# Optimization experiments

Measured on AMD Instinct MI355X. Metric: run time of the kernel, lower is better.

The kernel has to match this reference:

```python
import jax, jax.numpy as jnp
import numpy as np

N = 50000
E = 800000
F_IN = 256
HID = 96
N_CLS = 32
NEG_SLOPE = 0.2


def setup_inputs() -> dict:
    key = jax.random.key(0)
    ks = jax.random.split(key, 10)
    x = jax.random.normal(ks[0], (N, F_IN), dtype=jnp.float32)
    edge_index = jax.random.randint(ks[1], (2, E), 0, N, dtype=jnp.int64)
    s1 = 1.0 / np.sqrt(F_IN)
    s2 = 1.0 / np.sqrt(HID)
    return {
        "x": x,
        "edge_index": edge_index,
        "W1": jax.random.normal(ks[2], (F_IN, HID), dtype=jnp.float32) * s1,
        "a1_src": jax.random.normal(ks[3], (HID,), dtype=jnp.float32) * s2,
        "a1_dst": jax.random.normal(ks[4], (HID,), dtype=jnp.float32) * s2,
        "b1": jnp.zeros((HID,), dtype=jnp.float32),
        "W2": jax.random.normal(ks[5], (HID, N_CLS), dtype=jnp.float32) * s2,
        "a2_src": jax.random.normal(ks[6], (N_CLS,), dtype=jnp.float32) * (1.0 / np.sqrt(N_CLS)),
        "a2_dst": jax.random.normal(ks[7], (N_CLS,), dtype=jnp.float32) * (1.0 / np.sqrt(N_CLS)),
        "b2": jnp.zeros((N_CLS,), dtype=jnp.float32),
    }


def _gat_conv(x, src, dst, W, a_src, a_dst, b, n_nodes):
    # single-head GATConv (PyG defaults), self-loops already in src/dst
    h = x @ W                                  # [N, out]
    alpha_src = h @ a_src                      # [N]
    alpha_dst = h @ a_dst                      # [N]
    e = alpha_src[src] + alpha_dst[dst]        # [E'] edge logits (msg j->i: dst groups)
    e = jnp.where(e > 0, e, NEG_SLOPE * e)     # leaky_relu
    # segment softmax over edges grouped by destination node
    m = jax.ops.segment_max(e, dst, num_segments=n_nodes)
    ex = jnp.exp(e - m[dst])
    denom = jax.ops.segment_sum(ex, dst, num_segments=n_nodes)
    alpha = ex / denom[dst]                    # [E']
    out = jax.ops.segment_sum(alpha[:, None] * h[src], dst, num_segments=n_nodes)
    return out + b


def reference(x, edge_index, W1, a1_src, a1_dst, b1, W2, a2_src, a2_dst, b2):
    loops = jnp.arange(N, dtype=edge_index.dtype)
    src = jnp.concatenate([edge_index[0], loops])
    dst = jnp.concatenate([edge_index[1], loops])
    h = _gat_conv(x, src, dst, W1, a1_src, a1_dst, b1, N)
    h = jax.nn.elu(h)
    # dropout omitted (eval mode, training=False)
    out = _gat_conv(h, src, dst, W2, a2_src, a2_dst, b2, N)
    return jax.nn.log_softmax(out, axis=1)
```

## Files before the change

kernel.cpp:

```cpp
#include <hip/hip_runtime.h>
#include <cstdint>
#include <cstddef>

#define NNODES 50000
#define NEDGES 800000
#define MEDGES (NEDGES + NNODES)
#define FIN    256
#define HID    96
#define NCLS   32
#define NEG_SLOPE 0.2f

#define NBUCK  391
#define BCAP   3072

typedef unsigned int uint32;
typedef __attribute__((ext_vector_type(8))) short short8;
typedef __attribute__((ext_vector_type(4))) float f32x4;

__device__ __forceinline__ ushort bf_round(float f) {
    uint32 u = __float_as_uint(f);
    u += 0x7FFFu + ((u >> 16) & 1u);
    return (ushort)(u >> 16);
}
__device__ __forceinline__ uint32 pack_bf16x2(float a, float b) {
    return (uint32)bf_round(a) | ((uint32)bf_round(b) << 16);
}
__device__ __forceinline__ float bf_lo(uint32 u) { return __uint_as_float(u << 16); }
__device__ __forceinline__ float bf_hi(uint32 u) { return __uint_as_float(u & 0xFFFF0000u); }
__device__ __forceinline__ float lrelu(float t) { return (t > 0.f) ? t : NEG_SLOPE * t; }
__device__ __forceinline__ float af(int i) { return __int_as_float(i); }
__device__ __forceinline__ float elu_fast(float t) { return (t > 0.f) ? t : (__expf(t) - 1.f); }


__global__ __launch_bounds__(256) void packw_kernel(const float* __restrict__ W1,
                                                    ushort* __restrict__ W1p,
                                                    int* __restrict__ gcount) {
    int stride = gridDim.x * 256;
    for (int idx = blockIdx.x * 256 + threadIdx.x; idx < NBUCK; idx += stride)
        gcount[idx] = 0;
    for (int idx = blockIdx.x * 256 + threadIdx.x; idx < 6 * 8 * 64 * 8; idx += stride) {
        int j     = idx & 7;
        int lane  = (idx >> 3) & 63;
        int kstep = (idx >> 9) & 7;
        int ntile = idx >> 12;
        int k = kstep * 32 + ((lane >> 4) << 3) + j;
        int n = ntile * 16 + (lane & 15);
        W1p[idx] = bf_round(W1[(size_t)k * 96 + n]);
    }
}


__global__ __launch_bounds__(256) void bucket1_kernel(const int* __restrict__ ei,
                                                      int* __restrict__ gcount,
                                                      int* __restrict__ staging) {
    __shared__ int hist[NBUCK];
    __shared__ int base_sh[NBUCK];
    for (int i = threadIdx.x; i < NBUCK; i += 256) hist[i] = 0;
    __syncthreads();

    int v[8], rk[8], bk[8];
    int e0 = blockIdx.x * 2048;
#pragma unroll
    for (int i = 0; i < 8; ++i) {
        int e = e0 + i * 256 + threadIdx.x;
        if (e < MEDGES) {
            int s, d;
            if (e < NEDGES) { s = ei[e]; d = ei[NEDGES + e]; }
            else            { s = e - NEDGES; d = s; }
            bk[i] = d >> 7;
            v[i]  = s | ((d & 127) << 16);
            rk[i] = atomicAdd(&hist[bk[i]], 1);
        } else bk[i] = -1;
    }
    __syncthreads();
    for (int i = threadIdx.x; i < NBUCK; i += 256) {
        int c = hist[i];
        base_sh[i] = c ? atomicAdd(&gcount[i], c) : 0;
    }
    __syncthreads();
#pragma unroll
    for (int i = 0; i < 8; ++i) {
        if (bk[i] >= 0) {
            int pos = base_sh[bk[i]] + rk[i];
            if (pos < BCAP)
                staging[(size_t)bk[i] * BCAP + pos] = v[i];
        }
    }
}


__global__ __launch_bounds__(256) void b2gemm1_kernel(const int* __restrict__ staging,
                                                      const int* __restrict__ gcount,
                                                      int* __restrict__ rowptr,
                                                      int* __restrict__ esrc,
                                                      const float* __restrict__ x,
                                                      const ushort* __restrict__ W1p,
                                                      const float* __restrict__ a_src,
                                                      const float* __restrict__ a_dst,
                                                      ushort* __restrict__ h1,
                                                      float* __restrict__ as1,
                                                      float* __restrict__ ad1) {
    __shared__ int dcount[128];
    __shared__ int dincl[128];
    __shared__ int dexcl[128];
    __shared__ int fillc[128];
    __shared__ int red_s[256];

    if (blockIdx.x < NBUCK) {
        const int b = blockIdx.x;
        const int t = threadIdx.x;

        int pv = 0;
        for (int idx = t; idx < b; idx += 256) pv += gcount[idx];
        red_s[t] = pv;
        __syncthreads();
        for (int off2 = 128; off2; off2 >>= 1) {
            if (t < off2) red_s[t] += red_s[t + off2];
            __syncthreads();
        }
        const int ebase = red_s[0];
        const int cnt   = gcount[b];
        const int node0 = b << 7;
        const int* st   = staging + (size_t)b * BCAP;

        for (int i = t; i < 128; i += 256) { dcount[i] = 0; fillc[i] = 0; }
        __syncthreads();

        for (int i = t; i < cnt; i += 256)
            atomicAdd(&dcount[st[i] >> 16], 1);
        __syncthreads();

        if (t < 128) dincl[t] = dcount[t];
        __syncthreads();
        for (int off = 1; off < 128; off <<= 1) {
            int val = (t >= off && t < 128) ? dincl[t - off] : 0;
            __syncthreads();
            if (t < 128) dincl[t] += val;
            __syncthreads();
        }
        if (t < 128) {
            int excl = dincl[t] - dcount[t];
            dexcl[t] = excl;
            int node = node0 + t;
            if (node < NNODES) rowptr[node] = ebase + excl;
        }
        if (b == NBUCK - 1 && t == 0) rowptr[NNODES] = MEDGES;
        __syncthreads();

        for (int i = t; i < cnt; i += 256) {
            int v = st[i];
            int dd = v >> 16;
            int r = atomicAdd(&fillc[dd], 1);
            esrc[ebase + dexcl[dd] + r] = v & 0xFFFF;
        }
        return;
    }

    const int tid  = threadIdx.x;
    const int lane = tid & 63;
    const int wv   = tid >> 6;
    const int m    = lane & 15;
    const int quad = lane >> 4;
    const int node0 = (blockIdx.x - NBUCK) * 64;

    int arow = node0 + wv * 16 + m;
    if (arow >= NNODES) arow = NNODES - 1;
    const float* xr = x + (size_t)arow * FIN + quad * 8;

    const short8* Wp = (const short8*)W1p;

    f32x4 acc[6];
#pragma unroll
    for (int t = 0; t < 6; ++t) acc[t] = (f32x4){0.f, 0.f, 0.f, 0.f};

#pragma unroll
    for (int ks = 0; ks < 8; ++ks) {
        float4 v0 = *(const float4*)(xr + ks * 32);
        float4 v1 = *(const float4*)(xr + ks * 32 + 4);
        short8 a;
        a[0] = (short)bf_round(v0.x); a[1] = (short)bf_round(v0.y);
        a[2] = (short)bf_round(v0.z); a[3] = (short)bf_round(v0.w);
        a[4] = (short)bf_round(v1.x); a[5] = (short)bf_round(v1.y);
        a[6] = (short)bf_round(v1.z); a[7] = (short)bf_round(v1.w);
#pragma unroll
        for (int t = 0; t < 6; ++t) {
            short8 b = Wp[(t * 8 + ks) * 64 + lane];
            acc[t] = __builtin_amdgcn_mfma_f32_16x16x32_bf16(a, b, acc[t], 0, 0, 0);
        }
    }

    float as_reg[6], ad_reg[6];
#pragma unroll
    for (int t = 0; t < 6; ++t) {
        as_reg[t] = a_src[t * 16 + m];
        ad_reg[t] = a_dst[t * 16 + m];
    }

#pragma unroll
    for (int r = 0; r < 4; ++r) {
        int node = node0 + wv * 16 + quad * 4 + r;
        float ps = 0.f, pd = 0.f;
#pragma unroll
        for (int t = 0; t < 6; ++t) {
            ps += acc[t][r] * as_reg[t];
            pd += acc[t][r] * ad_reg[t];
        }
#pragma unroll
        for (int off = 1; off < 16; off <<= 1) {
            ps += __shfl_xor(ps, off);
            pd += __shfl_xor(pd, off);
        }
        if (node < NNODES) {
            ushort* hp = h1 + (size_t)node * 96 + m;
#pragma unroll
            for (int t = 0; t < 6; ++t) hp[t * 16] = bf_round(acc[t][r]);
            if (m == 0) { as1[node] = ps; ad1[node] = pd; }
        }
    }
}


__global__ __launch_bounds__(256) void agg96g2_kernel(const ushort* __restrict__ h,
                                                      const float* __restrict__ asrc,
                                                      const float* __restrict__ adst,
                                                      const float* __restrict__ bias,
                                                      const int* __restrict__ rowptr,
                                                      const int* __restrict__ esrc,
                                                      const float* __restrict__ W2,
                                                      const float* __restrict__ a2s,
                                                      const float* __restrict__ a2d,
                                                      uint32* __restrict__ h2b,
                                                      float* __restrict__ as2,
                                                      float* __restrict__ ad2) {
    __shared__ int2 sa[4][2][32];
    __shared__ __align__(16) float W2t[32 * 100];
    __shared__ __align__(16) float y_sh[4][2][96];

    for (int idx = threadIdx.x; idx < 96 * 32; idx += 256) {
        int c = idx & 31, k = idx >> 5;
        W2t[c * 100 + k] = W2[idx];
    }
    __syncthreads();

    const int wave = threadIdx.x >> 6;
    const int lane = threadIdx.x & 63;
    const int hf   = lane >> 5;
    const int fl32 = lane & 31;
    const int i = blockIdx.x * 8 + wave * 2 + hf;

    const int start = rowptr[i];
    const int deg   = rowptr[i + 1] - start;
    const float ad  = adst[i];
    const float a2s_v = a2s[fl32];
    const float a2d_v = a2d[fl32];
    const int fl    = (fl32 < 24) ? fl32 : 23;

    float acc0 = 0.f, acc1 = 0.f, acc2 = 0.f, acc3 = 0.f;

    if (deg <= 32) {
        bool valid = fl32 < deg;
        int s_reg = valid ? esrc[start + fl32] : 0;
        float e = valid ? lrelu(asrc[s_reg] + ad) : -1e30f;
        float mx = e;
#pragma unroll
        for (int off = 16; off; off >>= 1) mx = fmaxf(mx, __shfl_xor(mx, off));
        float ex = valid ? __expf(e - mx) : 0.f;
        float sum = ex;
#pragma unroll
        for (int off = 16; off; off >>= 1) sum += __shfl_xor(sum, off);
        sa[wave][hf][fl32] = make_int2(s_reg, __float_as_int(ex / sum));

        const int4* sap = (const int4*)&sa[wave][hf][0];

        for (int eb = 0; eb < deg; eb += 8) {
            int4 qa = sap[(eb >> 1) + 0];
            int4 qb = sap[(eb >> 1) + 1];
            int4 qc = sap[(eb >> 1) + 2];
            int4 qd = sap[(eb >> 1) + 3];
            const uint2* r0 = (const uint2*)(h + (size_t)qa.x * 96);
            const uint2* r1 = (const uint2*)(h + (size_t)qa.z * 96);
            const uint2* r2 = (const uint2*)(h + (size_t)qb.x * 96);
            const uint2* r3 = (const uint2*)(h + (size_t)qb.z * 96);
            const uint2* r4 = (const uint2*)(h + (size_t)qc.x * 96);
            const uint2* r5 = (const uint2*)(h + (size_t)qc.z * 96);
            const uint2* r6 = (const uint2*)(h + (size_t)qd.x * 96);
            const uint2* r7 = (const uint2*)(h + (size_t)qd.z * 96);
            uint2 u0 = r0[fl], u1 = r1[fl], u2 = r2[fl], u3 = r3[fl];
            uint2 u4 = r4[fl], u5 = r5[fl], u6 = r6[fl], u7 = r7[fl];
            float a0 = af(qa.y), a1 = af(qa.w), a2 = af(qb.y), a3 = af(qb.w);
            float a4 = af(qc.y), a5 = af(qc.w), a6 = af(qd.y), a7 = af(qd.w);
            acc0 += a0 * bf_lo(u0.x) + a1 * bf_lo(u1.x) + a2 * bf_lo(u2.x) + a3 * bf_lo(u3.x)
                  + a4 * bf_lo(u4.x) + a5 * bf_lo(u5.x) + a6 * bf_lo(u6.x) + a7 * bf_lo(u7.x);
            acc1 += a0 * bf_hi(u0.x) + a1 * bf_hi(u1.x) + a2 * bf_hi(u2.x) + a3 * bf_hi(u3.x)
                  + a4 * bf_hi(u4.x) + a5 * bf_hi(u5.x) + a6 * bf_hi(u6.x) + a7 * bf_hi(u7.x);
            acc2 += a0 * bf_lo(u0.y) + a1 * bf_lo(u1.y) + a2 * bf_lo(u2.y) + a3 * bf_lo(u3.y)
                  + a4 * bf_lo(u4.y) + a5 * bf_lo(u5.y) + a6 * bf_lo(u6.y) + a7 * bf_lo(u7.y);
            acc3 += a0 * bf_hi(u0.y) + a1 * bf_hi(u1.y) + a2 * bf_hi(u2.y) + a3 * bf_hi(u3.y)
                  + a4 * bf_hi(u4.y) + a5 * bf_hi(u5.y) + a6 * bf_hi(u6.y) + a7 * bf_hi(u7.y);
        }
    } else {
        float mx = -1e30f;
        for (int p = start + fl32; p < start + deg; p += 32)
            mx = fmaxf(mx, lrelu(asrc[esrc[p]] + ad));
#pragma unroll
        for (int off = 16; off; off >>= 1) mx = fmaxf(mx, __shfl_xor(mx, off));
        float sum = 0.f;
        for (int p = start + fl32; p < start + deg; p += 32)
            sum += __expf(lrelu(asrc[esrc[p]] + ad) - mx);
#pragma unroll
        for (int off = 16; off; off >>= 1) sum += __shfl_xor(sum, off);
        float inv = 1.f / sum;
        for (int e = 0; e < deg; ++e) {
            int s = esrc[start + e];
            float a = __expf(lrelu(asrc[s] + ad) - mx) * inv;
            uint2 u = ((const uint2*)(h + (size_t)s * 96))[fl];
            acc0 += a * bf_lo(u.x);
            acc1 += a * bf_hi(u.x);
            acc2 += a * bf_lo(u.y);
            acc3 += a * bf_hi(u.y);
        }
    }

    if (fl32 < 24) {
        float* yp = &y_sh[wave][hf][4 * fl32];
        yp[0] = elu_fast(acc0 + bias[4 * fl32 + 0]);
        yp[1] = elu_fast(acc1 + bias[4 * fl32 + 1]);
        yp[2] = elu_fast(acc2 + bias[4 * fl32 + 2]);
        yp[3] = elu_fast(acc3 + bias[4 * fl32 + 3]);
    }
    asm volatile("s_waitcnt lgkmcnt(0)" ::: "memory");

    const float* yrow = &y_sh[wave][hf][0];
    const float* wcol = W2t + fl32 * 100;
    float h2c = 0.f;
#pragma unroll
    for (int k = 0; k < 96; k += 4) {
        float4 yv = *(const float4*)(yrow + k);
        float4 wv = *(const float4*)(wcol + k);
        h2c = fmaf(yv.x, wv.x, h2c);
        h2c = fmaf(yv.y, wv.y, h2c);
        h2c = fmaf(yv.z, wv.z, h2c);
        h2c = fmaf(yv.w, wv.w, h2c);
    }

    float ps = h2c * a2s_v;
    float pd = h2c * a2d_v;
#pragma unroll
    for (int off = 1; off < 32; off <<= 1) {
        ps += __shfl_xor(ps, off);
        pd += __shfl_xor(pd, off);
    }
    float partner = __shfl_xor(h2c, 16);
    if (fl32 < 16)
        h2b[(size_t)i * 16 + fl32] = pack_bf16x2(h2c, partner);
    if (fl32 == 0) { as2[i] = ps; ad2[i] = pd; }
}


__global__ __launch_bounds__(256) void agg32_kernel(const uint32* __restrict__ h2b,
                                                    const float* __restrict__ asrc,
                                                    const float* __restrict__ adst,
                                                    const float* __restrict__ bias,
                                                    const int* __restrict__ rowptr,
                                                    const int* __restrict__ esrc,
                                                    float* __restrict__ out) {
    __shared__ int2 sa[4][2][32];
    const int wave = threadIdx.x >> 6;
    const int lane = threadIdx.x & 63;
    const int hf   = lane >> 5;
    const int fl32 = lane & 31;
    const int i = blockIdx.x * 8 + wave * 2 + hf;

    const int start = rowptr[i];
    const int deg   = rowptr[i + 1] - start;
    const float ad  = adst[i];
    const int g  = fl32 >> 3;
    const int fl = fl32 & 7;

    float acc[4];
#pragma unroll
    for (int j = 0; j < 4; ++j) acc[j] = 0.f;

    if (deg <= 32) {
        bool valid = fl32 < deg;
        int s_reg = valid ? esrc[start + fl32] : 0;
        float e = valid ? lrelu(asrc[s_reg] + ad) : -1e30f;
        float mx = e;
#pragma unroll
        for (int off = 16; off; off >>= 1) mx = fmaxf(mx, __shfl_xor(mx, off));
        float ex = valid ? __expf(e - mx) : 0.f;
        float sum = ex;
#pragma unroll
        for (int off = 16; off; off >>= 1) sum += __shfl_xor(sum, off);
        sa[wave][hf][fl32] = make_int2(s_reg, __float_as_int(ex / sum));

#pragma unroll 2
        for (int eb = 0; eb < deg; eb += 4) {
            int e0 = eb + g;
            int2 q = sa[wave][hf][(e0 < 32) ? e0 : 31];
            float a = (e0 < deg) ? af(q.y) : 0.f;
            const uint2* hr = (const uint2*)(h2b + (size_t)q.x * 16);
            uint2 u = hr[fl];
            acc[0] = fmaf(a, bf_lo(u.x), acc[0]);
            acc[1] = fmaf(a, bf_hi(u.x), acc[1]);
            acc[2] = fmaf(a, bf_lo(u.y), acc[2]);
            acc[3] = fmaf(a, bf_hi(u.y), acc[3]);
        }
    } else {
        float mx = -1e30f;
        for (int p = start + fl32; p < start + deg; p += 32)
            mx = fmaxf(mx, lrelu(asrc[esrc[p]] + ad));
#pragma unroll
        for (int off = 16; off; off >>= 1) mx = fmaxf(mx, __shfl_xor(mx, off));
        float sum = 0.f;
        for (int p = start + fl32; p < start + deg; p += 32)
            sum += __expf(lrelu(asrc[esrc[p]] + ad) - mx);
#pragma unroll
        for (int off = 16; off; off >>= 1) sum += __shfl_xor(sum, off);
        float inv = 1.f / sum;
        for (int p = start + g; p < start + deg; p += 4) {
            int s = esrc[p];
            float a = __expf(lrelu(asrc[s] + ad) - mx) * inv;
            const uint2* hr = (const uint2*)(h2b + (size_t)s * 16);
            uint2 u = hr[fl];
            acc[0] = fmaf(a, bf_lo(u.x), acc[0]);
            acc[1] = fmaf(a, bf_hi(u.x), acc[1]);
            acc[2] = fmaf(a, bf_lo(u.y), acc[2]);
            acc[3] = fmaf(a, bf_hi(u.y), acc[3]);
        }
    }

#pragma unroll
    for (int j = 0; j < 4; ++j) {
        acc[j] += __shfl_xor(acc[j], 8);
        acc[j] += __shfl_xor(acc[j], 16);
    }

    float z0 = acc[0] + bias[2 * fl];
    float z1 = acc[1] + bias[2 * fl + 16];
    float z2 = acc[2] + bias[2 * fl + 1];
    float z3 = acc[3] + bias[2 * fl + 17];
    float m2 = fmaxf(fmaxf(z0, z1), fmaxf(z2, z3));
#pragma unroll
    for (int off = 4; off; off >>= 1) m2 = fmaxf(m2, __shfl_xor(m2, off));
    float s2 = __expf(z0 - m2) + __expf(z1 - m2) + __expf(z2 - m2) + __expf(z3 - m2);
#pragma unroll
    for (int off = 4; off; off >>= 1) s2 += __shfl_xor(s2, off);
    float ls = m2 + __logf(s2);
    if (fl32 < 8) {
        float* op = out + (size_t)i * 32;
        op[2 * fl]      = z0 - ls;
        op[2 * fl + 16] = z1 - ls;
        op[2 * fl + 1]  = z2 - ls;
        op[2 * fl + 17] = z3 - ls;
    }
}


extern "C" void kernel_launch(void* const* d_in, const int* in_sizes, int n_in,
                              void* d_out, int out_size, void* d_ws, size_t ws_size,
                              hipStream_t stream) {
    const float* x   = (const float*)d_in[0];
    const int*   ei  = (const int*)d_in[1];
    const float* W1  = (const float*)d_in[2];
    const float* a1s = (const float*)d_in[3];
    const float* a1d = (const float*)d_in[4];
    const float* b1  = (const float*)d_in[5];
    const float* W2  = (const float*)d_in[6];
    const float* a2s = (const float*)d_in[7];
    const float* a2d = (const float*)d_in[8];
    const float* b2  = (const float*)d_in[9];
    float* out = (float*)d_out;

    size_t off = 0;
    auto alloc = [&](size_t bytes) {
        void* p = (char*)d_ws + off;
        off += (bytes + 255) & ~(size_t)255;
        return p;
    };
    ushort* h1    = (ushort*)alloc((size_t)NNODES * HID * 2);
    uint32* h2b   = (uint32*)alloc((size_t)NNODES * 16 * 4);
    int*  staging = (int*)alloc((size_t)NBUCK * BCAP * 4);
    float* as1    = (float*)alloc((size_t)NNODES * 4);
    float* ad1    = (float*)alloc((size_t)NNODES * 4);
    float* as2    = (float*)alloc((size_t)NNODES * 4);
    float* ad2    = (float*)alloc((size_t)NNODES * 4);
    int*   rowptr = (int*)alloc((size_t)(NNODES + 1) * 4);
    int*   esrc   = (int*)alloc((size_t)MEDGES * 4);
    ushort* W1p   = (ushort*)alloc((size_t)6 * 8 * 64 * 8 * 2);
    int*   gcount = (int*)alloc((size_t)NBUCK * 4);

    const int nbB1    = (MEDGES + 2047) / 2048;
    const int nbGemm  = (NNODES + 63) / 64;
    const int nbAggP  = NNODES / 8;

    packw_kernel<<<16, 256, 0, stream>>>(W1, W1p, gcount);
    bucket1_kernel<<<nbB1, 256, 0, stream>>>(ei, gcount, staging);
    b2gemm1_kernel<<<NBUCK + nbGemm, 256, 0, stream>>>(staging, gcount, rowptr, esrc,
                                                       x, W1p, a1s, a1d, h1, as1, ad1);
    agg96g2_kernel<<<nbAggP, 256, 0, stream>>>(h1, as1, ad1, b1, rowptr, esrc,
                                               W2, a2s, a2d, h2b, as2, ad2);
    agg32_kernel<<<nbAggP, 256, 0, stream>>>(h2b, as2, ad2, b2, rowptr, esrc, out);
}
```

Before: 207.4 us.

## Prefetch neighbor rows before softmax and W2 staging in agg96 kernel

```diff
diff --git a/kernel.cpp b/kernel.cpp
--- a/kernel.cpp
+++ b/kernel.cpp
@@ -220,6 +220,28 @@
 }
 
 
+#define LOADB(U, qa, qb) do { \
+    U[0] = ((const uint2*)(h + (size_t)(qa).x * 96))[fl]; \
+    U[1] = ((const uint2*)(h + (size_t)(qa).y * 96))[fl]; \
+    U[2] = ((const uint2*)(h + (size_t)(qa).z * 96))[fl]; \
+    U[3] = ((const uint2*)(h + (size_t)(qa).w * 96))[fl]; \
+    U[4] = ((const uint2*)(h + (size_t)(qb).x * 96))[fl]; \
+    U[5] = ((const uint2*)(h + (size_t)(qb).y * 96))[fl]; \
+    U[6] = ((const uint2*)(h + (size_t)(qb).z * 96))[fl]; \
+    U[7] = ((const uint2*)(h + (size_t)(qb).w * 96))[fl]; \
+} while (0)
+
+#define CONSUME(U, aL, aH) do { \
+    acc0 += (aL).x*bf_lo(U[0].x) + (aL).y*bf_lo(U[1].x) + (aL).z*bf_lo(U[2].x) + (aL).w*bf_lo(U[3].x) \
+          + (aH).x*bf_lo(U[4].x) + (aH).y*bf_lo(U[5].x) + (aH).z*bf_lo(U[6].x) + (aH).w*bf_lo(U[7].x); \
+    acc1 += (aL).x*bf_hi(U[0].x) + (aL).y*bf_hi(U[1].x) + (aL).z*bf_hi(U[2].x) + (aL).w*bf_hi(U[3].x) \
+          + (aH).x*bf_hi(U[4].x) + (aH).y*bf_hi(U[5].x) + (aH).z*bf_hi(U[6].x) + (aH).w*bf_hi(U[7].x); \
+    acc2 += (aL).x*bf_lo(U[0].y) + (aL).y*bf_lo(U[1].y) + (aL).z*bf_lo(U[2].y) + (aL).w*bf_lo(U[3].y) \
+          + (aH).x*bf_lo(U[4].y) + (aH).y*bf_lo(U[5].y) + (aH).z*bf_lo(U[6].y) + (aH).w*bf_lo(U[7].y); \
+    acc3 += (aL).x*bf_hi(U[0].y) + (aL).y*bf_hi(U[1].y) + (aL).z*bf_hi(U[2].y) + (aL).w*bf_hi(U[3].y) \
+          + (aH).x*bf_hi(U[4].y) + (aH).y*bf_hi(U[5].y) + (aH).z*bf_hi(U[6].y) + (aH).w*bf_hi(U[7].y); \
+} while (0)
+
 __global__ __launch_bounds__(256) void agg96g2_kernel(const ushort* __restrict__ h,
                                                       const float* __restrict__ asrc,
                                                       const float* __restrict__ adst,
@@ -232,15 +254,10 @@
                                                       uint32* __restrict__ h2b,
                                                       float* __restrict__ as2,
                                                       float* __restrict__ ad2) {
-    __shared__ int2 sa[4][2][32];
-    __shared__ __align__(16) float W2t[32 * 100];
+    __shared__ __align__(16) int   ss[4][2][32];
+    __shared__ __align__(16) float aa[4][2][32];
+    __shared__ __align__(16) float W2n[96 * 32];
     __shared__ __align__(16) float y_sh[4][2][96];
-
-    for (int idx = threadIdx.x; idx < 96 * 32; idx += 256) {
-        int c = idx & 31, k = idx >> 5;
-        W2t[c * 100 + k] = W2[idx];
-    }
-    __syncthreads();
 
     const int wave = threadIdx.x >> 6;
     const int lane = threadIdx.x & 63;
@@ -257,9 +274,32 @@
 
     float acc0 = 0.f, acc1 = 0.f, acc2 = 0.f, acc3 = 0.f;
 
-    if (deg <= 32) {
+    const bool small = (deg <= 32);
+    int s_reg = 0, nb = 0;
+    uint2 uA[8], uB[8];
+
+    if (small) {
         bool valid = fl32 < deg;
-        int s_reg = valid ? esrc[start + fl32] : 0;
+        s_reg = valid ? esrc[start + fl32] : 0;
+        ss[wave][hf][fl32] = s_reg;
+        nb = (deg + 7) >> 3;
+        const int4* ssp = (const int4*)&ss[wave][hf][0];
+        {
+            int4 qa = ssp[0], qb = ssp[1];
+            LOADB(uA, qa, qb);
+        }
+        if (nb > 1) {
+            int4 qa = ssp[2], qb = ssp[3];
+            LOADB(uB, qa, qb);
+        }
+    }
+
+    for (int idx = threadIdx.x; idx < 96 * 32; idx += 256)
+        W2n[idx] = W2[idx];
+    __syncthreads();
+
+    if (small) {
+        bool valid = fl32 < deg;
         float e = valid ? lrelu(asrc[s_reg] + ad) : -1e30f;
         float mx = e;
 #pragma unroll
@@ -268,36 +308,16 @@
         float sum = ex;
 #pragma unroll
         for (int off = 16; off; off >>= 1) sum += __shfl_xor(sum, off);
-        sa[wave][hf][fl32] = make_int2(s_reg, __float_as_int(ex / sum));
-
-        const int4* sap = (const int4*)&sa[wave][hf][0];
-
-        for (int eb = 0; eb < deg; eb += 8) {
-            int4 qa = sap[(eb >> 1) + 0];
-            int4 qb = sap[(eb >> 1) + 1];
-            int4 qc = sap[(eb >> 1) + 2];
-            int4 qd = sap[(eb >> 1) + 3];
-            const uint2* r0 = (const uint2*)(h + (size_t)qa.x * 96);
-            const uint2* r1 = (const uint2*)(h + (size_t)qa.z * 96);
-            const uint2* r2 = (const uint2*)(h + (size_t)qb.x * 96);
-            const uint2* r3 = (const uint2*)(h + (size_t)qb.z * 96);
-            const uint2* r4 = (const uint2*)(h + (size_t)qc.x * 96);
-            const uint2* r5 = (const uint2*)(h + (size_t)qc.z * 96);
-            const uint2* r6 = (const uint2*)(h + (size_t)qd.x * 96);
-            const uint2* r7 = (const uint2*)(h + (size_t)qd.z * 96);
-            uint2 u0 = r0[fl], u1 = r1[fl], u2 = r2[fl], u3 = r3[fl];
-            uint2 u4 = r4[fl], u5 = r5[fl], u6 = r6[fl], u7 = r7[fl];
-            float a0 = af(qa.y), a1 = af(qa.w), a2 = af(qb.y), a3 = af(qb.w);
-            float a4 = af(qc.y), a5 = af(qc.w), a6 = af(qd.y), a7 = af(qd.w);
-            acc0 += a0 * bf_lo(u0.x) + a1 * bf_lo(u1.x) + a2 * bf_lo(u2.x) + a3 * bf_lo(u3.x)
-                  + a4 * bf_lo(u4.x) + a5 * bf_lo(u5.x) + a6 * bf_lo(u6.x) + a7 * bf_lo(u7.x);
-            acc1 += a0 * bf_hi(u0.x) + a1 * bf_hi(u1.x) + a2 * bf_hi(u2.x) + a3 * bf_hi(u3.x)
-                  + a4 * bf_hi(u4.x) + a5 * bf_hi(u5.x) + a6 * bf_hi(u6.x) + a7 * bf_hi(u7.x);
-            acc2 += a0 * bf_lo(u0.y) + a1 * bf_lo(u1.y) + a2 * bf_lo(u2.y) + a3 * bf_lo(u3.y)
-                  + a4 * bf_lo(u4.y) + a5 * bf_lo(u5.y) + a6 * bf_lo(u6.y) + a7 * bf_lo(u7.y);
-            acc3 += a0 * bf_hi(u0.y) + a1 * bf_hi(u1.y) + a2 * bf_hi(u2.y) + a3 * bf_hi(u3.y)
-                  + a4 * bf_hi(u4.y) + a5 * bf_hi(u5.y) + a6 * bf_hi(u6.y) + a7 * bf_hi(u7.y);
-        }
+        aa[wave][hf][fl32] = ex / sum;
+        const float4* aap = (const float4*)&aa[wave][hf][0];
+        const int4*  ssp = (const int4*)&ss[wave][hf][0];
+
+        { float4 aL = aap[0], aH = aap[1]; CONSUME(uA, aL, aH); }
+        if (nb > 2) { int4 qa = ssp[4], qb = ssp[5]; LOADB(uA, qa, qb); }
+        if (nb > 1) { float4 aL = aap[2], aH = aap[3]; CONSUME(uB, aL, aH); }
+        if (nb > 3) { int4 qa = ssp[6], qb = ssp[7]; LOADB(uB, qa, qb); }
+        if (nb > 2) { float4 aL = aap[4], aH = aap[5]; CONSUME(uA, aL, aH); }
+        if (nb > 3) { float4 aL = aap[6], aH = aap[7]; CONSUME(uB, aL, aH); }
     } else {
         float mx = -1e30f;
         for (int p = start + fl32; p < start + deg; p += 32)
@@ -331,16 +351,14 @@
     asm volatile("s_waitcnt lgkmcnt(0)" ::: "memory");
 
     const float* yrow = &y_sh[wave][hf][0];
-    const float* wcol = W2t + fl32 * 100;
     float h2c = 0.f;
 #pragma unroll
-    for (int k = 0; k < 96; k += 4) {
-        float4 yv = *(const float4*)(yrow + k);
-        float4 wv = *(const float4*)(wcol + k);
-        h2c = fmaf(yv.x, wv.x, h2c);
-        h2c = fmaf(yv.y, wv.y, h2c);
-        h2c = fmaf(yv.z, wv.z, h2c);
-        h2c = fmaf(yv.w, wv.w, h2c);
+    for (int k4 = 0; k4 < 96; k4 += 4) {
+        float4 yv = *(const float4*)(yrow + k4);
+        h2c = fmaf(yv.x, W2n[(k4 + 0) * 32 + fl32], h2c);
+        h2c = fmaf(yv.y, W2n[(k4 + 1) * 32 + fl32], h2c);
+        h2c = fmaf(yv.z, W2n[(k4 + 2) * 32 + fl32], h2c);
+        h2c = fmaf(yv.w, W2n[(k4 + 3) * 32 + fl32], h2c);
     }
 
     float ps = h2c * a2s_v;
```

Result: slower. 215.3 us (+3.8%).
